# Kernel optimization log

Hardware: AMD Instinct MI355X
Metric: run time of the kernel (lower is better)

## Reference

```python
import jax, jax.numpy as jnp
import numpy as np

B, T, D = 64, 256, 1024
H, HS = 16, 64
FF = 4096
EPS = 1e-5


def _layernorm(x, g, b):
    mu = jnp.mean(x, axis=-1, keepdims=True)
    var = jnp.mean(jnp.square(x - mu), axis=-1, keepdims=True)
    return (x - mu) * jax.lax.rsqrt(var + EPS) * g + b


def setup_inputs() -> dict:
    key = jax.random.key(0)
    ks = jax.random.split(key, 12)
    s = 0.02
    return {
        "x": jax.random.normal(ks[0], (B, T, D), jnp.float32),
        "ln1_g": jnp.ones((D,), jnp.float32),
        "ln1_b": jnp.zeros((D,), jnp.float32),
        "Wq": jax.random.normal(ks[1], (H, D, HS), jnp.float32) * s,
        "Wk": jax.random.normal(ks[2], (H, D, HS), jnp.float32) * s,
        "Wv": jax.random.normal(ks[3], (H, D, HS), jnp.float32) * s,
        "Wproj": jax.random.normal(ks[4], (D, D), jnp.float32) * s,
        "bproj": jnp.zeros((D,), jnp.float32),
        "ln2_g": jnp.ones((D,), jnp.float32),
        "ln2_b": jnp.zeros((D,), jnp.float32),
        "W1": jax.random.normal(ks[5], (D, FF), jnp.float32) * s,
        "b1": jnp.zeros((FF,), jnp.float32),
        "W2": jax.random.normal(ks[6], (FF, D), jnp.float32) * s,
        "b2": jnp.zeros((D,), jnp.float32),
    }


def reference(x, ln1_g, ln1_b, Wq, Wk, Wv, Wproj, bproj, ln2_g, ln2_b, W1, b1, W2, b2):
    # x = ln1(x)
    h = _layernorm(x, ln1_g, ln1_b)
    # per-head Q/K/V projections, batched over heads
    q = jnp.einsum("btd,hde->bhte", h, Wq)
    k = jnp.einsum("btd,hde->bhte", h, Wk)
    v = jnp.einsum("btd,hde->bhte", h, Wv)
    # NOTE: source scales by C**-0.5 with C = input_size (D), not head_size
    scale = D ** -0.5
    scores = jnp.einsum("bhte,bhse->bhts", q, k) * scale
    causal = jnp.tril(jnp.ones((T, T), bool))
    scores = jnp.where(causal, scores, -jnp.inf)
    w = jax.nn.softmax(scores, axis=-1)  # dropout is identity in eval
    attn = jnp.einsum("bhts,bhse->bthe", w, v).reshape(x.shape[0], x.shape[1], H * HS)
    sa = attn @ Wproj + bproj
    # residual onto ln1 output (as written in source)
    y = h + sa
    h2 = _layernorm(y, ln2_g, ln2_b)
    ff = jax.nn.relu(h2 @ W1 + b1) @ W2 + b2
    return h2 + ff
```

## Files before the change

### kernel.cpp

```cpp
#include <hip/hip_runtime.h>

typedef __bf16 bf16x8 __attribute__((ext_vector_type(8)));
typedef float f32x4 __attribute__((ext_vector_type(4)));
typedef unsigned short ushort_t;

__device__ __forceinline__ ushort_t f2bf(float f) {
  unsigned int u = __float_as_uint(f);
  u += 0x7fffu + ((u >> 16) & 1u);
  return (ushort_t)(u >> 16);
}

__device__ __forceinline__ void gl_lds16(const ushort_t* g, const char* l) {
  __builtin_amdgcn_global_load_lds(
      (const __attribute__((address_space(1))) void*)g,
      (__attribute__((address_space(3))) void*)l, 16, 0, 0);
}

__global__ __launch_bounds__(256) void fill_k(float* __restrict__ p, long n, float v) {
  long i = (long)blockIdx.x * 256 + threadIdx.x;
  if (i < n) p[i] = v;
}

__global__ __launch_bounds__(256) void transpose_w(const float* __restrict__ in,
                                                   ushort_t* __restrict__ out,
                                                   int R, int C) {
  __shared__ float tile[32][33];
  const float* inb = in + (long)blockIdx.z * R * C;
  ushort_t* outb = out + (long)blockIdx.z * R * C;
  int r0 = blockIdx.x * 32, c0 = blockIdx.y * 32;
  int tx = threadIdx.x & 31, ty = threadIdx.x >> 5;
#pragma unroll
  for (int i = ty; i < 32; i += 8) tile[i][tx] = inb[(long)(r0 + i) * C + (c0 + tx)];
  __syncthreads();
#pragma unroll
  for (int i = ty; i < 32; i += 8) outb[(long)(c0 + i) * R + (r0 + tx)] = f2bf(tile[tx][i]);
}

__global__ __launch_bounds__(256) void ln_k(const float* __restrict__ x,
                                            const float* __restrict__ g,
                                            const float* __restrict__ b,
                                            float* __restrict__ outF,
                                            ushort_t* __restrict__ outU) {
  __shared__ float red[8];
  long row = blockIdx.x;
  int tid = threadIdx.x;
  float4 v = ((const float4*)(x + row * 1024))[tid];
  float s = v.x + v.y + v.z + v.w;
#pragma unroll
  for (int off = 32; off; off >>= 1) s += __shfl_xor(s, off);
  int w = tid >> 6;
  if ((tid & 63) == 0) red[w] = s;
  __syncthreads();
  float mean = (red[0] + red[1] + red[2] + red[3]) * (1.0f / 1024.0f);
  float dx = v.x - mean, dy = v.y - mean, dz = v.z - mean, dw = v.w - mean;
  float s2 = dx * dx + dy * dy + dz * dz + dw * dw;
#pragma unroll
  for (int off = 32; off; off >>= 1) s2 += __shfl_xor(s2, off);
  if ((tid & 63) == 0) red[4 + w] = s2;
  __syncthreads();
  float var = (red[4] + red[5] + red[6] + red[7]) * (1.0f / 1024.0f);
  float rstd = rsqrtf(var + 1e-5f);
  int c = tid * 4;
  float o0 = dx * rstd * g[c + 0] + b[c + 0];
  float o1 = dy * rstd * g[c + 1] + b[c + 1];
  float o2 = dz * rstd * g[c + 2] + b[c + 2];
  float o3 = dw * rstd * g[c + 3] + b[c + 3];
  ((float4*)(outF + row * 1024))[tid] = make_float4(o0, o1, o2, o3);
  ushort4 u;
  u.x = f2bf(o0); u.y = f2bf(o1); u.z = f2bf(o2); u.w = f2bf(o3);
  ((ushort4*)(outU + row * 1024))[tid] = u;
}

template <int EPI>
__global__ __launch_bounds__(512, 2) void gemm256(const ushort_t* __restrict__ A,
                                                  const ushort_t* __restrict__ Bt,
                                                  int M, int N, int K, int NBC,
                                                  const float* __restrict__ bias,
                                                  const float* res, float* outF,
                                                  ushort_t* __restrict__ outU) {
  __shared__ __align__(16) char lds[98304];
  const int tid = threadIdx.x;
  const int lane = tid & 63;
  const int w = tid >> 6;
  const int wr = w >> 2, wc = w & 3;
  const int g = lane >> 4, lr = lane & 15;
  const int cpx = gridDim.x >> 3;
  const int wg = (blockIdx.x & 7) * cpx + (blockIdx.x >> 3);
  const long m0 = (long)(wg / NBC) * 256;
  const long n0 = (long)(wg % NBC) * 256;
  const int u = (tid & 7) ^ ((tid >> 3) & 7);
  const int rbase = ((tid >> 3) << 1) | (u >> 2);
  const int gcol = (u & 3) * 8;
  const ushort_t* sA0 = A + (m0 + rbase) * (long)K + gcol;
  const ushort_t* sA1 = A + (m0 + 128 + rbase) * (long)K + gcol;
  const ushort_t* sB0 = Bt + (n0 + rbase) * (long)K + gcol;
  const ushort_t* sB1 = Bt + (n0 + 128 + rbase) * (long)K + gcol;
  const int swz = (((lr & 1) << 2) + g) ^ (lr >> 1);
  const int aRd = wr * 8192 + (lr >> 1) * 128 + swz * 16;
  const int bRd = 49152 + wc * 4096 + (lr >> 1) * 128 + swz * 16;
  const int dA = tid * 16;
  const int dB = 49152 + tid * 16;
  const int NT = K >> 5;

  f32x4 acc[8][4] = {};

  gl_lds16(sA0, lds + 0 + dA);
  gl_lds16(sA1, lds + 8192 + dA);
  gl_lds16(sB0, lds + 0 + dB);
  gl_lds16(sB1, lds + 8192 + dB);
  gl_lds16(sA0 + 32, lds + 16384 + dA);
  gl_lds16(sA1 + 32, lds + 16384 + 8192 + dA);
  gl_lds16(sB0 + 32, lds + 16384 + dB);
  gl_lds16(sB1 + 32, lds + 16384 + 8192 + dB);
  asm volatile("s_waitcnt vmcnt(4)" ::: "memory");
  __builtin_amdgcn_s_barrier();

  int ro = 0, wo = 32768;
  for (int t = 0; t < NT; ++t) {
    const bool st = (t + 2 < NT);
    const long ks = (long)(t + 2) * 32;
    bf16x8 fa[4], fb[4];
#pragma unroll
    for (int mf = 0; mf < 4; ++mf)
      fa[mf] = *(const bf16x8*)(lds + ro + aRd + mf * 1024);
#pragma unroll
    for (int nf = 0; nf < 4; ++nf)
      fb[nf] = *(const bf16x8*)(lds + ro + bRd + nf * 1024);
    if (st) {
      gl_lds16(sA0 + ks, lds + wo + dA);
      gl_lds16(sA1 + ks, lds + wo + 8192 + dA);
    }
    __builtin_amdgcn_s_barrier();
    asm volatile("s_waitcnt lgkmcnt(0)" ::: "memory");
    __builtin_amdgcn_s_setprio(1);
#pragma unroll
    for (int mf = 0; mf < 4; ++mf)
#pragma unroll
      for (int nf = 0; nf < 4; ++nf)
        acc[mf][nf] = __builtin_amdgcn_mfma_f32_16x16x32_bf16(fa[mf], fb[nf], acc[mf][nf], 0, 0, 0);
    __builtin_amdgcn_s_setprio(0);
    __builtin_amdgcn_s_barrier();
#pragma unroll
    for (int mf = 0; mf < 4; ++mf)
      fa[mf] = *(const bf16x8*)(lds + ro + aRd + (4 + mf) * 1024);
    if (st) {
      gl_lds16(sB0 + ks, lds + wo + dB);
      gl_lds16(sB1 + ks, lds + wo + 8192 + dB);
    }
    __builtin_amdgcn_s_barrier();
    asm volatile("s_waitcnt lgkmcnt(0)" ::: "memory");
    __builtin_amdgcn_s_setprio(1);
#pragma unroll
    for (int mf = 0; mf < 4; ++mf)
#pragma unroll
      for (int nf = 0; nf < 4; ++nf)
        acc[4 + mf][nf] = __builtin_amdgcn_mfma_f32_16x16x32_bf16(fa[mf], fb[nf], acc[4 + mf][nf], 0, 0, 0);
    __builtin_amdgcn_s_setprio(0);
    if (st) asm volatile("s_waitcnt vmcnt(4)" ::: "memory");
    else    asm volatile("s_waitcnt vmcnt(0)" ::: "memory");
    __builtin_amdgcn_s_barrier();
    ro += 16384; if (ro == 49152) ro = 0;
    wo += 16384; if (wo == 49152) wo = 0;
  }

#pragma unroll
  for (int mf = 0; mf < 8; ++mf)
#pragma unroll
    for (int nf = 0; nf < 4; ++nf)
#pragma unroll
      for (int r = 0; r < 4; ++r) {
        long row = m0 + wr * 128 + mf * 16 + g * 4 + r;
        long col = n0 + wc * 64 + nf * 16 + lr;
        float v = acc[mf][nf][r];
        if constexpr (EPI == 0) {
          long bb = row >> 8, tt = row & 255, hh = col >> 6, e = col & 63;
          outU[(((bb * 16 + hh) * 256 + tt) << 6) + e] = f2bf(v);
        } else if constexpr (EPI == 1) {
          long bb = row >> 8, tt = row & 255, hh = col >> 6, e = col & 63;
          outU[(((bb * 16 + hh) * 64 + e) << 8) + tt] = f2bf(v);
        } else if constexpr (EPI == 2) {
          long i = row * N + col;
          outF[i] = v + bias[col] + res[i];
        } else {
          outU[row * N + col] = f2bf(fmaxf(v + bias[col], 0.0f));
        }
      }
}

__global__ __launch_bounds__(64) void attn_k(const ushort_t* __restrict__ q,
                                             const ushort_t* __restrict__ k,
                                             const ushort_t* __restrict__ vt,
                                             ushort_t* __restrict__ ao) {
  __shared__ __align__(16) ushort_t Ps[64][40];
  const int lane = threadIdx.x;
  const int g = lane >> 4, lr = lane & 15;
  const int blk = blockIdx.x;
  const int q4 = blk & 3;
  const int bh = blk >> 2;
  const int bb = bh >> 4, hh = bh & 15;
  const int q0 = q4 * 64;
  const ushort_t* qb = q + (long)bh * 256 * 64;
  const ushort_t* kb = k + (long)bh * 256 * 64;
  const ushort_t* vb = vt + (long)bh * 64 * 256;
  bf16x8 qf[4][2];
#pragma unroll
  for (int m = 0; m < 4; m++)
#pragma unroll
    for (int ks = 0; ks < 2; ks++)
      qf[m][ks] = *(const bf16x8*)(qb + (q0 + m * 16 + lr) * 64 + ks * 32 + g * 8);
  f32x4 o[4][4] = {};
  float mrow[4][4], lrow[4][4];
#pragma unroll
  for (int m = 0; m < 4; m++)
#pragma unroll
    for (int r = 0; r < 4; r++) { mrow[m][r] = -__builtin_inff(); lrow[m][r] = 0.0f; }
  const float scale = 0.03125f;
  const int nkb = q0 / 32 + 2;
  for (int kbk = 0; kbk < nkb; kbk++) {
    f32x4 s[4][2] = {};
#pragma unroll
    for (int ks = 0; ks < 2; ks++) {
      bf16x8 kf[2];
#pragma unroll
      for (int n = 0; n < 2; n++)
        kf[n] = *(const bf16x8*)(kb + (kbk * 32 + n * 16 + lr) * 64 + ks * 32 + g * 8);
#pragma unroll
      for (int m = 0; m < 4; m++)
#pragma unroll
        for (int n = 0; n < 2; n++)
          s[m][n] = __builtin_amdgcn_mfma_f32_16x16x32_bf16(qf[m][ks], kf[n], s[m][n], 0, 0, 0);
    }
#pragma unroll
    for (int m = 0; m < 4; m++)
#pragma unroll
      for (int n = 0; n < 2; n++)
#pragma unroll
        for (int r = 0; r < 4; r++) {
          int row = q0 + m * 16 + g * 4 + r;
          int col = kbk * 32 + n * 16 + lr;
          float v = s[m][n][r] * scale;
          s[m][n][r] = (col <= row) ? v : -1e30f;
        }
#pragma unroll
    for (int m = 0; m < 4; m++)
#pragma unroll
      for (int r = 0; r < 4; r++) {
        float mx = fmaxf(s[m][0][r], s[m][1][r]);
#pragma unroll
        for (int off = 8; off; off >>= 1) mx = fmaxf(mx, __shfl_xor(mx, off));
        float mn = fmaxf(mrow[m][r], mx);
        float alpha = __expf(mrow[m][r] - mn);
        mrow[m][r] = mn;
        float rs = 0.0f;
#pragma unroll
        for (int n = 0; n < 2; n++) {
          float p = __expf(s[m][n][r] - mn);
          s[m][n][r] = p;
          rs += p;
        }
#pragma unroll
        for (int off = 8; off; off >>= 1) rs += __shfl_xor(rs, off);
        lrow[m][r] = lrow[m][r] * alpha + rs;
#pragma unroll
        for (int n = 0; n < 4; n++) o[m][n][r] *= alpha;
      }
#pragma unroll
    for (int m = 0; m < 4; m++)
#pragma unroll
      for (int n = 0; n < 2; n++)
#pragma unroll
        for (int r = 0; r < 4; r++)
          Ps[m * 16 + g * 4 + r][n * 16 + lr] = f2bf(s[m][n][r]);
    __syncthreads();
    bf16x8 vf[4];
#pragma unroll
    for (int n = 0; n < 4; n++)
      vf[n] = *(const bf16x8*)(vb + (n * 16 + lr) * 256 + kbk * 32 + g * 8);
#pragma unroll
    for (int m = 0; m < 4; m++) {
      bf16x8 pa = *(const bf16x8*)&Ps[m * 16 + lr][g * 8];
#pragma unroll
      for (int n = 0; n < 4; n++)
        o[m][n] = __builtin_amdgcn_mfma_f32_16x16x32_bf16(pa, vf[n], o[m][n], 0, 0, 0);
    }
    __syncthreads();
  }
#pragma unroll
  for (int m = 0; m < 4; m++)
#pragma unroll
    for (int r = 0; r < 4; r++) {
      float inv = 1.0f / lrow[m][r];
      long t = q0 + m * 16 + g * 4 + r;
#pragma unroll
      for (int n = 0; n < 4; n++) {
        long e = n * 16 + lr;
        ao[((long)bb * 256 + t) * 1024 + hh * 64 + e] = f2bf(o[m][n][r] * inv);
      }
    }
}

extern "C" void kernel_launch(void* const* d_in, const int* in_sizes, int n_in,
                              void* d_out, int out_size, void* d_ws, size_t ws_size,
                              hipStream_t stream) {
  const float* x     = (const float*)d_in[0];
  const float* ln1g  = (const float*)d_in[1];
  const float* ln1b  = (const float*)d_in[2];
  const float* Wq    = (const float*)d_in[3];
  const float* Wk    = (const float*)d_in[4];
  const float* Wv    = (const float*)d_in[5];
  const float* Wproj = (const float*)d_in[6];
  const float* bproj = (const float*)d_in[7];
  const float* ln2g  = (const float*)d_in[8];
  const float* ln2b  = (const float*)d_in[9];
  const float* W1    = (const float*)d_in[10];
  const float* b1    = (const float*)d_in[11];
  const float* W2    = (const float*)d_in[12];
  const float* b2    = (const float*)d_in[13];

  const long NEED = 184L << 20;
  if (ws_size < (size_t)NEED) {
    fill_k<<<(out_size + 255) / 256, 256, 0, stream>>>((float*)d_out, out_size,
                                                       (float)(ws_size >> 20));
    return;
  }

  char* ws = (char*)d_ws;
  const long MB = 1 << 20;
  ushort_t* wqt = (ushort_t*)(ws + 0 * MB);
  ushort_t* wkt = (ushort_t*)(ws + 2 * MB);
  ushort_t* wvt = (ushort_t*)(ws + 4 * MB);
  ushort_t* wpt = (ushort_t*)(ws + 6 * MB);
  ushort_t* w1t = (ushort_t*)(ws + 8 * MB);
  ushort_t* w2t = (ushort_t*)(ws + 16 * MB);
  ushort_t* hb  = (ushort_t*)(ws + 24 * MB);
  ushort_t* qbf = (ushort_t*)(ws + 56 * MB);
  ushort_t* kbf = (ushort_t*)(ws + 88 * MB);
  ushort_t* vtb = (ushort_t*)(ws + 120 * MB);
  ushort_t* atb = (ushort_t*)(ws + 152 * MB);
  ushort_t* ff1 = (ushort_t*)(ws + 56 * MB);
  float*    yf  = (float*)d_out;

  transpose_w<<<dim3(32, 2, 16), 256, 0, stream>>>(Wq, wqt, 1024, 64);
  transpose_w<<<dim3(32, 2, 16), 256, 0, stream>>>(Wk, wkt, 1024, 64);
  transpose_w<<<dim3(32, 2, 16), 256, 0, stream>>>(Wv, wvt, 1024, 64);
  transpose_w<<<dim3(32, 32, 1), 256, 0, stream>>>(Wproj, wpt, 1024, 1024);
  transpose_w<<<dim3(32, 128, 1), 256, 0, stream>>>(W1, w1t, 1024, 4096);
  transpose_w<<<dim3(128, 32, 1), 256, 0, stream>>>(W2, w2t, 4096, 1024);

  ln_k<<<16384, 256, 0, stream>>>(x, ln1g, ln1b, yf, hb);
  gemm256<0><<<256, 512, 0, stream>>>(hb, wqt, 16384, 1024, 1024, 4, nullptr, nullptr, nullptr, qbf);
  gemm256<0><<<256, 512, 0, stream>>>(hb, wkt, 16384, 1024, 1024, 4, nullptr, nullptr, nullptr, kbf);
  gemm256<1><<<256, 512, 0, stream>>>(hb, wvt, 16384, 1024, 1024, 4, nullptr, nullptr, nullptr, vtb);
  attn_k<<<4096, 64, 0, stream>>>(qbf, kbf, vtb, atb);
  gemm256<2><<<256, 512, 0, stream>>>(atb, wpt, 16384, 1024, 1024, 4, bproj, yf, yf, nullptr);
  ln_k<<<16384, 256, 0, stream>>>(yf, ln2g, ln2b, yf, hb);
  gemm256<3><<<1024, 512, 0, stream>>>(hb, w1t, 16384, 4096, 1024, 16, b1, nullptr, nullptr, ff1);
  gemm256<2><<<256, 512, 0, stream>>>(ff1, w2t, 16384, 1024, 4096, 4, b2, yf, yf, nullptr);
}
```

Measured before the change: 676.2 us.

## Restructure GEMM mainloop to 64-deep double-buffered K tiles and fuse QKV GEMMs

The GEMM main loop now stages 64-wide K slices per iteration into two 64 KB LDS buffers instead of a three-stage ring of 32-wide slices. It also uses a new XOR swizzle and splits the MFMA work into four phases with B and A fragment reloads in between. Separately, the Q, K and V projections become one GEMM with N=3072, whose epilogue routes each column range to the Q, K or transposed-V buffer. This relies on the transposed weights being stored contiguously. The aim is fewer barriers per unit of K, better latency hiding and fewer launches, but 128 KB of LDS per block likely limits the CU to one resident block.

```diff
diff --git a/kernel.cpp b/kernel.cpp
--- a/kernel.cpp
+++ b/kernel.cpp
@@ -77,8 +77,10 @@
                                                   int M, int N, int K, int NBC,
                                                   const float* __restrict__ bias,
                                                   const float* res, float* outF,
-                                                  ushort_t* __restrict__ outU) {
-  __shared__ __align__(16) char lds[98304];
+                                                  ushort_t* __restrict__ outU,
+                                                  ushort_t* __restrict__ outU2,
+                                                  ushort_t* __restrict__ outU3) {
+  __shared__ __align__(16) char lds[131072];
   const int tid = threadIdx.x;
   const int lane = tid & 63;
   const int w = tid >> 6;
@@ -88,79 +90,103 @@
   const int wg = (blockIdx.x & 7) * cpx + (blockIdx.x >> 3);
   const long m0 = (long)(wg / NBC) * 256;
   const long n0 = (long)(wg % NBC) * 256;
-  const int u = (tid & 7) ^ ((tid >> 3) & 7);
-  const int rbase = ((tid >> 3) << 1) | (u >> 2);
-  const int gcol = (u & 3) * 8;
-  const ushort_t* sA0 = A + (m0 + rbase) * (long)K + gcol;
-  const ushort_t* sA1 = A + (m0 + 128 + rbase) * (long)K + gcol;
-  const ushort_t* sB0 = Bt + (n0 + rbase) * (long)K + gcol;
-  const ushort_t* sB1 = Bt + (n0 + 128 + rbase) * (long)K + gcol;
-  const int swz = (((lr & 1) << 2) + g) ^ (lr >> 1);
-  const int aRd = wr * 8192 + (lr >> 1) * 128 + swz * 16;
-  const int bRd = 49152 + wc * 4096 + (lr >> 1) * 128 + swz * 16;
+  const int srow = tid >> 3;
+  const int sslot = (tid & 7) ^ (srow & 7);
+  const ushort_t* sA = A + (m0 + srow) * (long)K + sslot * 8;
+  const ushort_t* sB = Bt + (n0 + srow) * (long)K + sslot * 8;
   const int dA = tid * 16;
-  const int dB = 49152 + tid * 16;
-  const int NT = K >> 5;
+  const int dB = 32768 + tid * 16;
+  const int abase = (wr * 128 + lr) * 128;
+  const int bbase = 32768 + (wc * 64 + lr) * 128;
+  const int s0 = g ^ (lr & 7);
+  const int s1 = (4 + g) ^ (lr & 7);
+  const int NT = K >> 6;
 
   f32x4 acc[8][4] = {};
 
-  gl_lds16(sA0, lds + 0 + dA);
-  gl_lds16(sA1, lds + 8192 + dA);
-  gl_lds16(sB0, lds + 0 + dB);
-  gl_lds16(sB1, lds + 8192 + dB);
-  gl_lds16(sA0 + 32, lds + 16384 + dA);
-  gl_lds16(sA1 + 32, lds + 16384 + 8192 + dA);
-  gl_lds16(sB0 + 32, lds + 16384 + dB);
-  gl_lds16(sB1 + 32, lds + 16384 + 8192 + dB);
-  asm volatile("s_waitcnt vmcnt(4)" ::: "memory");
-  __builtin_amdgcn_s_barrier();
-
-  int ro = 0, wo = 32768;
+#pragma unroll
+  for (int j = 0; j < 4; ++j) gl_lds16(sA + (long)j * 64 * K, lds + j * 8192 + dA);
+#pragma unroll
+  for (int j = 0; j < 4; ++j) gl_lds16(sB + (long)j * 64 * K, lds + j * 8192 + dB);
+
+  bf16x8 aR[4][2], bR[4][2];
+  int c = 0;
   for (int t = 0; t < NT; ++t) {
-    const bool st = (t + 2 < NT);
-    const long ks = (long)(t + 2) * 32;
-    bf16x8 fa[4], fb[4];
+    const char* rb = lds + c;
+    if (t + 1 < NT) {
+      const long ko = (long)(t + 1) * 64;
+      const int d = c ^ 65536;
+#pragma unroll
+      for (int j = 0; j < 4; ++j) gl_lds16(sA + ko + (long)j * 64 * K, lds + d + j * 8192 + dA);
+#pragma unroll
+      for (int j = 0; j < 4; ++j) gl_lds16(sB + ko + (long)j * 64 * K, lds + d + j * 8192 + dB);
+      asm volatile("s_waitcnt vmcnt(8)" ::: "memory");
+    } else {
+      asm volatile("s_waitcnt vmcnt(0)" ::: "memory");
+    }
+    __builtin_amdgcn_s_barrier();
+    __builtin_amdgcn_sched_barrier(0);
+#pragma unroll
+    for (int mf = 0; mf < 4; ++mf) {
+      aR[mf][0] = *(const bf16x8*)(rb + abase + mf * 2048 + s0 * 16);
+      aR[mf][1] = *(const bf16x8*)(rb + abase + mf * 2048 + s1 * 16);
+    }
+#pragma unroll
+    for (int nf = 0; nf < 2; ++nf) {
+      bR[nf][0] = *(const bf16x8*)(rb + bbase + nf * 2048 + s0 * 16);
+      bR[nf][1] = *(const bf16x8*)(rb + bbase + nf * 2048 + s1 * 16);
+    }
+    __builtin_amdgcn_s_setprio(1);
 #pragma unroll
     for (int mf = 0; mf < 4; ++mf)
-      fa[mf] = *(const bf16x8*)(lds + ro + aRd + mf * 1024);
-#pragma unroll
-    for (int nf = 0; nf < 4; ++nf)
-      fb[nf] = *(const bf16x8*)(lds + ro + bRd + nf * 1024);
-    if (st) {
-      gl_lds16(sA0 + ks, lds + wo + dA);
-      gl_lds16(sA1 + ks, lds + wo + 8192 + dA);
-    }
-    __builtin_amdgcn_s_barrier();
-    asm volatile("s_waitcnt lgkmcnt(0)" ::: "memory");
+#pragma unroll
+      for (int nf = 0; nf < 2; ++nf) {
+        acc[mf][nf] = __builtin_amdgcn_mfma_f32_16x16x32_bf16(aR[mf][0], bR[nf][0], acc[mf][nf], 0, 0, 0);
+        acc[mf][nf] = __builtin_amdgcn_mfma_f32_16x16x32_bf16(aR[mf][1], bR[nf][1], acc[mf][nf], 0, 0, 0);
+      }
+    __builtin_amdgcn_s_setprio(0);
+    __builtin_amdgcn_s_barrier();
+#pragma unroll
+    for (int nf = 2; nf < 4; ++nf) {
+      bR[nf][0] = *(const bf16x8*)(rb + bbase + nf * 2048 + s0 * 16);
+      bR[nf][1] = *(const bf16x8*)(rb + bbase + nf * 2048 + s1 * 16);
+    }
     __builtin_amdgcn_s_setprio(1);
 #pragma unroll
     for (int mf = 0; mf < 4; ++mf)
 #pragma unroll
-      for (int nf = 0; nf < 4; ++nf)
-        acc[mf][nf] = __builtin_amdgcn_mfma_f32_16x16x32_bf16(fa[mf], fb[nf], acc[mf][nf], 0, 0, 0);
+      for (int nf = 2; nf < 4; ++nf) {
+        acc[mf][nf] = __builtin_amdgcn_mfma_f32_16x16x32_bf16(aR[mf][0], bR[nf][0], acc[mf][nf], 0, 0, 0);
+        acc[mf][nf] = __builtin_amdgcn_mfma_f32_16x16x32_bf16(aR[mf][1], bR[nf][1], acc[mf][nf], 0, 0, 0);
+      }
     __builtin_amdgcn_s_setprio(0);
     __builtin_amdgcn_s_barrier();
 #pragma unroll
+    for (int mf = 0; mf < 4; ++mf) {
+      aR[mf][0] = *(const bf16x8*)(rb + abase + (4 + mf) * 2048 + s0 * 16);
+      aR[mf][1] = *(const bf16x8*)(rb + abase + (4 + mf) * 2048 + s1 * 16);
+    }
+    __builtin_amdgcn_s_setprio(1);
+#pragma unroll
     for (int mf = 0; mf < 4; ++mf)
-      fa[mf] = *(const bf16x8*)(lds + ro + aRd + (4 + mf) * 1024);
-    if (st) {
-      gl_lds16(sB0 + ks, lds + wo + dB);
-      gl_lds16(sB1 + ks, lds + wo + 8192 + dB);
-    }
-    __builtin_amdgcn_s_barrier();
-    asm volatile("s_waitcnt lgkmcnt(0)" ::: "memory");
+#pragma unroll
+      for (int nf = 2; nf < 4; ++nf) {
+        acc[4 + mf][nf] = __builtin_amdgcn_mfma_f32_16x16x32_bf16(aR[mf][0], bR[nf][0], acc[4 + mf][nf], 0, 0, 0);
+        acc[4 + mf][nf] = __builtin_amdgcn_mfma_f32_16x16x32_bf16(aR[mf][1], bR[nf][1], acc[4 + mf][nf], 0, 0, 0);
+      }
+    __builtin_amdgcn_s_setprio(0);
+    __builtin_amdgcn_s_barrier();
     __builtin_amdgcn_s_setprio(1);
 #pragma unroll
     for (int mf = 0; mf < 4; ++mf)
 #pragma unroll
-      for (int nf = 0; nf < 4; ++nf)
-        acc[4 + mf][nf] = __builtin_amdgcn_mfma_f32_16x16x32_bf16(fa[mf], fb[nf], acc[4 + mf][nf], 0, 0, 0);
+      for (int nf = 0; nf < 2; ++nf) {
+        acc[4 + mf][nf] = __builtin_amdgcn_mfma_f32_16x16x32_bf16(aR[mf][0], bR[nf][0], acc[4 + mf][nf], 0, 0, 0);
+        acc[4 + mf][nf] = __builtin_amdgcn_mfma_f32_16x16x32_bf16(aR[mf][1], bR[nf][1], acc[4 + mf][nf], 0, 0, 0);
+      }
     __builtin_amdgcn_s_setprio(0);
-    if (st) asm volatile("s_waitcnt vmcnt(4)" ::: "memory");
-    else    asm volatile("s_waitcnt vmcnt(0)" ::: "memory");
-    __builtin_amdgcn_s_barrier();
-    ro += 16384; if (ro == 49152) ro = 0;
-    wo += 16384; if (wo == 49152) wo = 0;
+    __builtin_amdgcn_s_barrier();
+    c ^= 65536;
   }
 
 #pragma unroll
@@ -172,17 +198,20 @@
         long row = m0 + wr * 128 + mf * 16 + g * 4 + r;
         long col = n0 + wc * 64 + nf * 16 + lr;
         float v = acc[mf][nf][r];
-        if constexpr (EPI == 0) {
-          long bb = row >> 8, tt = row & 255, hh = col >> 6, e = col & 63;
-          outU[(((bb * 16 + hh) * 256 + tt) << 6) + e] = f2bf(v);
-        } else if constexpr (EPI == 1) {
-          long bb = row >> 8, tt = row & 255, hh = col >> 6, e = col & 63;
-          outU[(((bb * 16 + hh) * 64 + e) << 8) + tt] = f2bf(v);
-        } else if constexpr (EPI == 2) {
+        if constexpr (EPI == 2) {
           long i = row * N + col;
           outF[i] = v + bias[col] + res[i];
+        } else if constexpr (EPI == 3) {
+          outU[row * N + col] = f2bf(fmaxf(v + bias[col], 0.0f));
         } else {
-          outU[row * N + col] = f2bf(fmaxf(v + bias[col], 0.0f));
+          long bb2 = row >> 8, tt = row & 255;
+          long p = col >> 10, cc = col & 1023, hh = cc >> 6, e = cc & 63;
+          if (p == 0)
+            outU[(((bb2 * 16 + hh) * 256 + tt) << 6) + e] = f2bf(v);
+          else if (p == 1)
+            outU2[(((bb2 * 16 + hh) * 256 + tt) << 6) + e] = f2bf(v);
+          else
+            outU3[(((bb2 * 16 + hh) * 64 + e) << 8) + tt] = f2bf(v);
         }
       }
 }
@@ -348,12 +377,14 @@
   transpose_w<<<dim3(128, 32, 1), 256, 0, stream>>>(W2, w2t, 4096, 1024);
 
   ln_k<<<16384, 256, 0, stream>>>(x, ln1g, ln1b, yf, hb);
-  gemm256<0><<<256, 512, 0, stream>>>(hb, wqt, 16384, 1024, 1024, 4, nullptr, nullptr, nullptr, qbf);
-  gemm256<0><<<256, 512, 0, stream>>>(hb, wkt, 16384, 1024, 1024, 4, nullptr, nullptr, nullptr, kbf);
-  gemm256<1><<<256, 512, 0, stream>>>(hb, wvt, 16384, 1024, 1024, 4, nullptr, nullptr, nullptr, vtb);
+  gemm256<4><<<768, 512, 0, stream>>>(hb, wqt, 16384, 3072, 1024, 12,
+                                      nullptr, nullptr, nullptr, qbf, kbf, vtb);
   attn_k<<<4096, 64, 0, stream>>>(qbf, kbf, vtb, atb);
-  gemm256<2><<<256, 512, 0, stream>>>(atb, wpt, 16384, 1024, 1024, 4, bproj, yf, yf, nullptr);
+  gemm256<2><<<256, 512, 0, stream>>>(atb, wpt, 16384, 1024, 1024, 4,
+                                      bproj, yf, yf, nullptr, nullptr, nullptr);
   ln_k<<<16384, 256, 0, stream>>>(yf, ln2g, ln2b, yf, hb);
-  gemm256<3><<<1024, 512, 0, stream>>>(hb, w1t, 16384, 4096, 1024, 16, b1, nullptr, nullptr, ff1);
-  gemm256<2><<<256, 512, 0, stream>>>(ff1, w2t, 16384, 1024, 4096, 4, b2, yf, yf, nullptr);
-}
+  gemm256<3><<<1024, 512, 0, stream>>>(hb, w1t, 16384, 4096, 1024, 16,
+                                       b1, nullptr, nullptr, ff1, nullptr, nullptr);
+  gemm256<2><<<256, 512, 0, stream>>>(ff1, w2t, 16384, 1024, 4096, 4,
+                                      b2, yf, yf, nullptr, nullptr, nullptr);
+}
```

Measured after the change: 693.1 us. +2.5%, slower.
